# Performance work log

Measured on AMD Instinct MI355X. Metric: run time of the kernel, lower is better.

The kernel has to match this reference:

```python
import jax, jax.numpy as jnp
import numpy as np

N_NODES = 50000
N_EDGES = 1600000
D_IN = 128
D_HID = 128
D_OUT = 128


def setup_inputs() -> dict:
    key = jax.random.key(0)
    ks = jax.random.split(key, 12)
    s = 0.05
    return {
        "x": jax.random.normal(ks[0], (N_NODES, D_IN), jnp.float32),
        "src": jax.random.randint(ks[1], (N_EDGES,), 0, N_NODES),
        "dst": jax.random.randint(ks[2], (N_EDGES,), 0, N_NODES),
        "W_neigh1": jax.random.normal(ks[3], (D_HID, D_IN), jnp.float32) * s,
        "W_self1": jax.random.normal(ks[4], (D_HID, D_IN), jnp.float32) * s,
        "b_self1": jnp.zeros((D_HID,), jnp.float32),
        "W_neigh2": jax.random.normal(ks[5], (D_HID, D_HID), jnp.float32) * s,
        "W_self2": jax.random.normal(ks[6], (D_HID, D_HID), jnp.float32) * s,
        "b_self2": jnp.zeros((D_HID,), jnp.float32),
        "W_neigh3": jax.random.normal(ks[7], (D_OUT, D_HID), jnp.float32) * s,
        "W_self3": jax.random.normal(ks[8], (D_OUT, D_HID), jnp.float32) * s,
        "b_self3": jnp.zeros((D_OUT,), jnp.float32),
    }


def _sage_mean(h, src, dst, inv_deg, W_neigh, W_self, b_self):
    # DGL SAGEConv 'mean': fc_self(h) + fc_neigh(mean of in-neighbor feats)
    # zero in-degree nodes get zero neighbor term (inv_deg = 0 there is avoided
    # by clamping degree to >=1, sum is 0 anyway).
    neigh_sum = jax.ops.segment_sum(h[src], dst, num_segments=h.shape[0])  # [N, d]
    h_neigh = neigh_sum * inv_deg  # [N, d]
    return h @ W_self.T + b_self + h_neigh @ W_neigh.T


def reference(x, src, dst, W_neigh1, W_self1, b_self1, W_neigh2, W_self2, b_self2, W_neigh3, W_self3, b_self3):
    n = x.shape[0]
    deg = jax.ops.segment_sum(jnp.ones((src.shape[0],), x.dtype), dst, num_segments=n)
    inv_deg = (1.0 / jnp.maximum(deg, 1.0))[:, None]  # [N, 1]
    h = jax.nn.relu(_sage_mean(x, src, dst, inv_deg, W_neigh1, W_self1, b_self1))
    h = jax.nn.relu(_sage_mean(h, src, dst, inv_deg, W_neigh2, W_self2, b_self2))
    h = _sage_mean(h, src, dst, inv_deg, W_neigh3, W_self3, b_self3)
    return h
```

## Files before the change

kernel.cpp:

```cpp
#include <hip/hip_runtime.h>


constexpr int N_NODES = 50000;
constexpr int N_EDGES = 1600000;
constexpr int D = 128;

constexpr int NBUCK = 392;
constexpr int BCAP  = 6144;
constexpr int EPB   = 4096;
constexpr int CS_BLOCKS = (N_EDGES + EPB - 1) / EPB;
constexpr int GC_STRIDE = 16;

typedef __bf16 bf16x8 __attribute__((ext_vector_type(8)));
typedef float f32x4 __attribute__((ext_vector_type(4)));
union U8 { bf16x8 v; __bf16 e[8]; };

__global__ void zero1(int* __restrict__ a, int n) {
    int i = blockIdx.x * blockDim.x + threadIdx.x;
    if (i < n) a[i] = 0;
}

__global__ __launch_bounds__(256) void bucket_count_scatter(
        const int* __restrict__ dst, const int* __restrict__ src,
        int* __restrict__ gcursor, int* __restrict__ bucketbuf) {
    __shared__ int hcnt[NBUCK];
    __shared__ int hbase[NBUCK];
    const int tid = threadIdx.x;
    for (int i = tid; i < NBUCK; i += 256) hcnt[i] = 0;
    __syncthreads();

    const int e0 = blockIdx.x * EPB;
    int d[16], lp[16];
    #pragma unroll
    for (int t = 0; t < 16; ++t) {
        const int e = e0 + t * 256 + tid;
        if (e < N_EDGES) {
            d[t] = dst[e];
            lp[t] = atomicAdd(&hcnt[d[t] >> 7], 1);
        } else {
            d[t] = 0; lp[t] = -1;
        }
    }
    __syncthreads();

    for (int i = tid; i < NBUCK; i += 256) {
        const int c = hcnt[i];
        hbase[i] = c ? atomicAdd(&gcursor[i * GC_STRIDE], c) : 0;
    }
    __syncthreads();

    #pragma unroll
    for (int t = 0; t < 16; ++t) {
        const int e = e0 + t * 256 + tid;
        if (e < N_EDGES) {
            const int s  = src[e];
            const int bk = d[t] >> 7;
            const int p  = hbase[bk] + lp[t];
            if (p < BCAP)
                bucketbuf[bk * BCAP + p] = ((d[t] & 127) << 16) | s;
        }
    }
}

__global__ void bucket_scan(const int* __restrict__ gcursor,
                            int* __restrict__ bucket_base,
                            int* __restrict__ row_ptr) {
    __shared__ int wsum[8], wpre[8];
    const int t = threadIdx.x;
    const int lane = t & 63, w = t >> 6;
    int v = 0;
    if (t < NBUCK) { v = gcursor[t * GC_STRIDE]; if (v > BCAP) v = BCAP; }
    int x = v;
    #pragma unroll
    for (int off = 1; off < 64; off <<= 1) {
        int tt = __shfl_up(x, off, 64);
        if (lane >= off) x += tt;
    }
    if (lane == 63) wsum[w] = x;
    __syncthreads();
    if (t < 8) {
        int s = wsum[t], y = s;
        #pragma unroll
        for (int off = 1; off < 8; off <<= 1) {
            int tt = __shfl_up(y, off, 64);
            if (t >= off) y += tt;
        }
        wpre[t] = y - s;
    }
    __syncthreads();
    if (t < NBUCK) bucket_base[t] = wpre[w] + (x - v);
    if (t == 0) row_ptr[N_NODES] = N_EDGES;
}

__global__ __launch_bounds__(256) void bucket_csr(
        const int* __restrict__ gcursor, const int* __restrict__ bucket_base,
        const int* __restrict__ bucketbuf, int* __restrict__ row_ptr,
        float* __restrict__ inv_deg, int* __restrict__ esrc) {
    __shared__ int h[128];
    __shared__ int cur[128];
    __shared__ int s0tot;
    const int bk = blockIdx.x, tid = threadIdx.x;
    int cnt = gcursor[bk * GC_STRIDE];
    if (cnt > BCAP) cnt = BCAP;
    const int base = bucket_base[bk];
    if (tid < 128) h[tid] = 0;
    __syncthreads();

    const int* bb = bucketbuf + (size_t)bk * BCAP;
    for (int i = tid; i < cnt; i += 256) atomicAdd(&h[bb[i] >> 16], 1);
    __syncthreads();

    const int c = (tid < 128) ? h[tid] : 0;
    int x = c;
    const int lane = tid & 63;
    #pragma unroll
    for (int off = 1; off < 64; off <<= 1) {
        int tt = __shfl_up(x, off, 64);
        if (lane >= off) x += tt;
    }
    if (tid == 63) s0tot = x;
    __syncthreads();
    const int excl = x - c + ((tid >= 64 && tid < 128) ? s0tot : 0);
    if (tid < 128) {
        cur[tid] = excl;
        const int node = (bk << 7) + tid;
        if (node < N_NODES) {
            row_ptr[node] = base + excl;
            inv_deg[node] = 1.0f / fmaxf((float)c, 1.0f);
        }
    }
    __syncthreads();

    for (int i = tid; i < cnt; i += 256) {
        const int p = bb[i];
        esrc[base + atomicAdd(&cur[p >> 16], 1)] = p & 0xFFFF;
    }
}

__global__ void pack_w(const float* __restrict__ w0, const float* __restrict__ w1,
                       const float* __restrict__ w2, const float* __restrict__ w3,
                       const float* __restrict__ w4, const float* __restrict__ w5,
                       __bf16* __restrict__ outbase) {
    const float* ws[6] = {w0, w1, w2, w3, w4, w5};
    const float* W = ws[blockIdx.y];
    __bf16* o = outbase + (size_t)blockIdx.y * 32768;
    int idx = blockIdx.x * 256 + threadIdx.x;
    int t = idx & 7;
    int lane = (idx >> 3) & 63;
    int ks = (idx >> 9) & 3;
    int jt = idx >> 11;
    int j = jt * 16 + (lane & 15);
    int k = ks * 32 + (lane >> 4) * 8 + t;
    float w = W[j * D + k];
    __bf16 hi = (__bf16)w;
    o[idx] = hi;
    o[16384 + idx] = (__bf16)(w - (float)hi);
}

__global__ __launch_bounds__(256) void dual_gemm(
        const float* __restrict__ h, const __bf16* __restrict__ Bs,
        const __bf16* __restrict__ Bn, const float* __restrict__ bias,
        float* __restrict__ y_self, __bf16* __restrict__ z) {
    const int wave = threadIdx.x >> 6;
    const int lane = threadIdx.x & 63;
    const int tile = blockIdx.x * 4 + wave;
    if (tile >= N_NODES / 16) return;
    const int n0 = tile * 16;
    const int row = n0 + (lane & 15);
    const int koff = (lane >> 4) * 8;

    U8 ahi[4], alo[4];
    #pragma unroll
    for (int ks = 0; ks < 4; ++ks) {
        const float* p = h + (size_t)row * D + ks * 32 + koff;
        float f[8];
        *(f32x4*)&f[0] = *(const f32x4*)p;
        *(f32x4*)&f[4] = *(const f32x4*)(p + 4);
        #pragma unroll
        for (int t = 0; t < 8; ++t) {
            __bf16 hi = (__bf16)f[t];
            ahi[ks].e[t] = hi;
            alo[ks].e[t] = (__bf16)(f[t] - (float)hi);
        }
    }

    const int jcol = lane & 15;
    const int r0 = (lane >> 4) * 4;

    #pragma unroll 2
    for (int jt = 0; jt < 8; ++jt) {
        f32x4 accS = {0.f, 0.f, 0.f, 0.f};
        f32x4 accN = {0.f, 0.f, 0.f, 0.f};
        #pragma unroll
        for (int ks = 0; ks < 4; ++ks) {
            const size_t off = (((size_t)jt * 4 + ks) * 64 + lane) * 8;
            bf16x8 wsh = *(const bf16x8*)(Bs + off);
            bf16x8 wsl = *(const bf16x8*)(Bs + 16384 + off);
            bf16x8 wnh = *(const bf16x8*)(Bn + off);
            bf16x8 wnl = *(const bf16x8*)(Bn + 16384 + off);
            accS = __builtin_amdgcn_mfma_f32_16x16x32_bf16(ahi[ks].v, wsh, accS, 0, 0, 0);
            accS = __builtin_amdgcn_mfma_f32_16x16x32_bf16(alo[ks].v, wsh, accS, 0, 0, 0);
            accS = __builtin_amdgcn_mfma_f32_16x16x32_bf16(ahi[ks].v, wsl, accS, 0, 0, 0);
            accN = __builtin_amdgcn_mfma_f32_16x16x32_bf16(ahi[ks].v, wnh, accN, 0, 0, 0);
            accN = __builtin_amdgcn_mfma_f32_16x16x32_bf16(alo[ks].v, wnh, accN, 0, 0, 0);
            accN = __builtin_amdgcn_mfma_f32_16x16x32_bf16(ahi[ks].v, wnl, accN, 0, 0, 0);
        }
        const int j = jt * 16 + jcol;
        const float bj = bias[j];
        #pragma unroll
        for (int r = 0; r < 4; ++r) {
            const size_t n = n0 + r0 + r;
            y_self[n * D + j] = accS[r] + bj;
            z[n * D + j] = (__bf16)accN[r];
        }
    }
}

__global__ __launch_bounds__(256) void agg_add(
        const __bf16* __restrict__ z, const int* __restrict__ esrc,
        const int* __restrict__ row_ptr, const float* __restrict__ inv_deg,
        const float* __restrict__ y_self, float* __restrict__ out, int do_relu) {
    const int n = blockIdx.x * 4 + (threadIdx.x >> 6);
    const int lane = threadIdx.x & 63;
    const int s = lane >> 4;
    const int c = lane & 15;
    const int r0 = row_ptr[n], r1 = row_ptr[n + 1];

    float acc[8] = {0.f, 0.f, 0.f, 0.f, 0.f, 0.f, 0.f, 0.f};
    int e = r0 + s;
    for (; e + 12 < r1; e += 16) {
        int i0 = esrc[e], i1 = esrc[e + 4], i2 = esrc[e + 8], i3 = esrc[e + 12];
        U8 v0, v1, v2, v3;
        v0.v = *(const bf16x8*)(z + (size_t)i0 * D + c * 8);
        v1.v = *(const bf16x8*)(z + (size_t)i1 * D + c * 8);
        v2.v = *(const bf16x8*)(z + (size_t)i2 * D + c * 8);
        v3.v = *(const bf16x8*)(z + (size_t)i3 * D + c * 8);
        #pragma unroll
        for (int t = 0; t < 8; ++t)
            acc[t] += ((float)v0.e[t] + (float)v1.e[t]) + ((float)v2.e[t] + (float)v3.e[t]);
    }
    for (; e < r1; e += 4) {
        U8 v0;
        v0.v = *(const bf16x8*)(z + (size_t)esrc[e] * D + c * 8);
        #pragma unroll
        for (int t = 0; t < 8; ++t) acc[t] += (float)v0.e[t];
    }
    #pragma unroll
    for (int t = 0; t < 8; ++t) acc[t] += __shfl_down(acc[t], 32, 64);
    #pragma unroll
    for (int t = 0; t < 8; ++t) acc[t] += __shfl_down(acc[t], 16, 64);

    if (lane < 16) {
        const float idg = inv_deg[n];
        const float* yp = y_self + (size_t)n * D + c * 8;
        f32x4 y0 = *(const f32x4*)yp;
        f32x4 y1 = *(const f32x4*)(yp + 4);
        float o[8];
        #pragma unroll
        for (int t = 0; t < 4; ++t) o[t] = y0[t] + acc[t] * idg;
        #pragma unroll
        for (int t = 0; t < 4; ++t) o[4 + t] = y1[t] + acc[4 + t] * idg;
        if (do_relu) {
            #pragma unroll
            for (int t = 0; t < 8; ++t) o[t] = fmaxf(o[t], 0.f);
        }
        float* op = out + (size_t)n * D + c * 8;
        *(f32x4*)op = *(f32x4*)&o[0];
        *(f32x4*)(op + 4) = *(f32x4*)&o[4];
    }
}

extern "C" void kernel_launch(void* const* d_in, const int* in_sizes, int n_in,
                              void* d_out, int out_size, void* d_ws, size_t ws_size,
                              hipStream_t stream) {
    const float* x   = (const float*)d_in[0];
    const int* src   = (const int*)d_in[1];
    const int* dst   = (const int*)d_in[2];
    const float* Wn1 = (const float*)d_in[3];
    const float* Ws1 = (const float*)d_in[4];
    const float* b1  = (const float*)d_in[5];
    const float* Wn2 = (const float*)d_in[6];
    const float* Ws2 = (const float*)d_in[7];
    const float* b2  = (const float*)d_in[8];
    const float* Wn3 = (const float*)d_in[9];
    const float* Ws3 = (const float*)d_in[10];
    const float* b3  = (const float*)d_in[11];
    float* out = (float*)d_out;

    char* w = (char*)d_ws;
    float* inv_deg     = (float*)w;             w += 50176 * 4;
    int* row_ptr       = (int*)w;               w += 50432 * 4;
    int* gcursor       = (int*)w;               w += NBUCK * GC_STRIDE * 4;
    int* bucket_base   = (int*)w;               w += 512 * 4;
    int* esrc          = (int*)w;               w += (size_t)N_EDGES * 4;
    __bf16* Bpk        = (__bf16*)w;            w += 6 * 32768 * 2;
    __bf16* zbuf       = (__bf16*)w;            w += (size_t)50176 * D * 2;
    float* bufA        = (float*)w;

    int* bucketbuf = (int*)zbuf;

    const __bf16* PWs1 = Bpk + 0 * 32768, *PWn1 = Bpk + 1 * 32768;
    const __bf16* PWs2 = Bpk + 2 * 32768, *PWn2 = Bpk + 3 * 32768;
    const __bf16* PWs3 = Bpk + 4 * 32768, *PWn3 = Bpk + 5 * 32768;

    zero1<<<(NBUCK * GC_STRIDE + 255) / 256, 256, 0, stream>>>(gcursor, NBUCK * GC_STRIDE);
    bucket_count_scatter<<<CS_BLOCKS, 256, 0, stream>>>(dst, src, gcursor, bucketbuf);
    bucket_scan<<<1, 512, 0, stream>>>(gcursor, bucket_base, row_ptr);
    bucket_csr<<<NBUCK, 256, 0, stream>>>(gcursor, bucket_base, bucketbuf,
                                          row_ptr, inv_deg, esrc);

    pack_w<<<dim3(64, 6), 256, 0, stream>>>(Ws1, Wn1, Ws2, Wn2, Ws3, Wn3, Bpk);

    const int ggrid = (N_NODES / 16 + 3) / 4;
    const int agrid = N_NODES / 4;

    dual_gemm<<<ggrid, 256, 0, stream>>>(x, PWs1, PWn1, b1, bufA, zbuf);
    agg_add<<<agrid, 256, 0, stream>>>(zbuf, esrc, row_ptr, inv_deg, bufA, bufA, 1);

    dual_gemm<<<ggrid, 256, 0, stream>>>(bufA, PWs2, PWn2, b2, out, zbuf);
    agg_add<<<agrid, 256, 0, stream>>>(zbuf, esrc, row_ptr, inv_deg, out, out, 1);

    dual_gemm<<<ggrid, 256, 0, stream>>>(out, PWs3, PWn3, b3, bufA, zbuf);
    agg_add<<<agrid, 256, 0, stream>>>(zbuf, esrc, row_ptr, inv_deg, bufA, out, 0);
}
```

Before: 378.9 us.

## Tile neighbor aggregation by source-node range for cache locality

The CSR build now sorts each destination's edges into 8 source-range tiles of 8192 nodes and stores per-(node, tile) offsets instead of a plain row_ptr. The new aggregation kernel loops over the tiles in its outer loop, so all waves gather from the same slice of z at roughly the same time. The aim is for that slice to stay cache-resident and cut random HBM traffic. Each wave now handles 14 nodes with half-waves and a fixed grid of 1024 blocks. In exchange there are many short divergent per-tile loops and fewer waves in flight.

```diff
diff --git a/kernel.cpp b/kernel.cpp
--- a/kernel.cpp
+++ b/kernel.cpp
@@ -10,6 +10,11 @@
 constexpr int EPB   = 4096;
 constexpr int CS_BLOCKS = (N_EDGES + EPB - 1) / EPB;
 constexpr int GC_STRIDE = 16;
+
+constexpr int NT  = 8;
+constexpr int TSH = 13;
+constexpr int AGG_BLOCKS = 1024;
+constexpr int PW = 14;
 
 typedef __bf16 bf16x8 __attribute__((ext_vector_type(8)));
 typedef float f32x4 __attribute__((ext_vector_type(4)));
@@ -63,8 +68,7 @@
 }
 
 __global__ void bucket_scan(const int* __restrict__ gcursor,
-                            int* __restrict__ bucket_base,
-                            int* __restrict__ row_ptr) {
+                            int* __restrict__ bucket_base) {
     __shared__ int wsum[8], wpre[8];
     const int t = threadIdx.x;
     const int lane = t & 63, w = t >> 6;
@@ -89,51 +93,66 @@
     }
     __syncthreads();
     if (t < NBUCK) bucket_base[t] = wpre[w] + (x - v);
-    if (t == 0) row_ptr[N_NODES] = N_EDGES;
 }
 
 __global__ __launch_bounds__(256) void bucket_csr(
         const int* __restrict__ gcursor, const int* __restrict__ bucket_base,
-        const int* __restrict__ bucketbuf, int* __restrict__ row_ptr,
+        const int* __restrict__ bucketbuf, int* __restrict__ tp,
         float* __restrict__ inv_deg, int* __restrict__ esrc) {
-    __shared__ int h[128];
-    __shared__ int cur[128];
-    __shared__ int s0tot;
+    __shared__ int h[1024];
+    __shared__ int cur[1024];
+    __shared__ int wsum[4], wpre[4];
     const int bk = blockIdx.x, tid = threadIdx.x;
     int cnt = gcursor[bk * GC_STRIDE];
     if (cnt > BCAP) cnt = BCAP;
     const int base = bucket_base[bk];
-    if (tid < 128) h[tid] = 0;
+    #pragma unroll
+    for (int k = 0; k < 4; ++k) h[tid * 4 + k] = 0;
     __syncthreads();
 
     const int* bb = bucketbuf + (size_t)bk * BCAP;
-    for (int i = tid; i < cnt; i += 256) atomicAdd(&h[bb[i] >> 16], 1);
-    __syncthreads();
-
-    const int c = (tid < 128) ? h[tid] : 0;
-    int x = c;
-    const int lane = tid & 63;
+    for (int i = tid; i < cnt; i += 256) {
+        const int p = bb[i];
+        atomicAdd(&h[((p >> 16) << 3) | ((p & 0xFFFF) >> TSH)], 1);
+    }
+    __syncthreads();
+
+    if (tid < 128) {
+        int dg = 0;
+        #pragma unroll
+        for (int k = 0; k < 8; ++k) dg += h[tid * 8 + k];
+        inv_deg[bk * 128 + tid] = 1.0f / fmaxf((float)dg, 1.0f);
+    }
+
+    int v0 = h[tid * 4], v1 = h[tid * 4 + 1], v2 = h[tid * 4 + 2], v3 = h[tid * 4 + 3];
+    const int s = v0 + v1 + v2 + v3;
+    int x = s;
+    const int lane = tid & 63, w = tid >> 6;
     #pragma unroll
     for (int off = 1; off < 64; off <<= 1) {
         int tt = __shfl_up(x, off, 64);
         if (lane >= off) x += tt;
     }
-    if (tid == 63) s0tot = x;
-    __syncthreads();
-    const int excl = x - c + ((tid >= 64 && tid < 128) ? s0tot : 0);
-    if (tid < 128) {
-        cur[tid] = excl;
-        const int node = (bk << 7) + tid;
-        if (node < N_NODES) {
-            row_ptr[node] = base + excl;
-            inv_deg[node] = 1.0f / fmaxf((float)c, 1.0f);
-        }
-    }
+    if (lane == 63) wsum[w] = x;
+    __syncthreads();
+    if (tid == 0) {
+        int a = 0;
+        #pragma unroll
+        for (int k = 0; k < 4; ++k) { wpre[k] = a; a += wsum[k]; }
+    }
+    __syncthreads();
+    const int e0 = wpre[w] + (x - s);
+    const int e1 = e0 + v0, e2 = e1 + v1, e3 = e2 + v2;
+    cur[tid * 4] = e0; cur[tid * 4 + 1] = e1;
+    cur[tid * 4 + 2] = e2; cur[tid * 4 + 3] = e3;
+    int* tpo = tp + (size_t)bk * 1024 + tid * 4;
+    tpo[0] = base + e0; tpo[1] = base + e1; tpo[2] = base + e2; tpo[3] = base + e3;
     __syncthreads();
 
     for (int i = tid; i < cnt; i += 256) {
         const int p = bb[i];
-        esrc[base + atomicAdd(&cur[p >> 16], 1)] = p & 0xFFFF;
+        const int f = ((p >> 16) << 3) | ((p & 0xFFFF) >> TSH);
+        esrc[base + atomicAdd(&cur[f], 1)] = p & 0xFFFF;
     }
 }
 
@@ -216,57 +235,70 @@
     }
 }
 
-__global__ __launch_bounds__(256) void agg_add(
+__global__ __launch_bounds__(256, 4) void agg_tiled(
         const __bf16* __restrict__ z, const int* __restrict__ esrc,
-        const int* __restrict__ row_ptr, const float* __restrict__ inv_deg,
+        const int* __restrict__ tp, const float* __restrict__ inv_deg,
         const float* __restrict__ y_self, float* __restrict__ out, int do_relu) {
-    const int n = blockIdx.x * 4 + (threadIdx.x >> 6);
+    const int wid = (blockIdx.x * 256 + threadIdx.x) >> 6;
     const int lane = threadIdx.x & 63;
-    const int s = lane >> 4;
-    const int c = lane & 15;
-    const int r0 = row_ptr[n], r1 = row_ptr[n + 1];
-
-    float acc[8] = {0.f, 0.f, 0.f, 0.f, 0.f, 0.f, 0.f, 0.f};
-    int e = r0 + s;
-    for (; e + 12 < r1; e += 16) {
-        int i0 = esrc[e], i1 = esrc[e + 4], i2 = esrc[e + 8], i3 = esrc[e + 12];
-        U8 v0, v1, v2, v3;
-        v0.v = *(const bf16x8*)(z + (size_t)i0 * D + c * 8);
-        v1.v = *(const bf16x8*)(z + (size_t)i1 * D + c * 8);
-        v2.v = *(const bf16x8*)(z + (size_t)i2 * D + c * 8);
-        v3.v = *(const bf16x8*)(z + (size_t)i3 * D + c * 8);
-        #pragma unroll
-        for (int t = 0; t < 8; ++t)
-            acc[t] += ((float)v0.e[t] + (float)v1.e[t]) + ((float)v2.e[t] + (float)v3.e[t]);
-    }
-    for (; e < r1; e += 4) {
-        U8 v0;
-        v0.v = *(const bf16x8*)(z + (size_t)esrc[e] * D + c * 8);
-        #pragma unroll
-        for (int t = 0; t < 8; ++t) acc[t] += (float)v0.e[t];
-    }
-    #pragma unroll
-    for (int t = 0; t < 8; ++t) acc[t] += __shfl_down(acc[t], 32, 64);
-    #pragma unroll
-    for (int t = 0; t < 8; ++t) acc[t] += __shfl_down(acc[t], 16, 64);
-
-    if (lane < 16) {
-        const float idg = inv_deg[n];
-        const float* yp = y_self + (size_t)n * D + c * 8;
-        f32x4 y0 = *(const f32x4*)yp;
-        f32x4 y1 = *(const f32x4*)(yp + 4);
-        float o[8];
-        #pragma unroll
-        for (int t = 0; t < 4; ++t) o[t] = y0[t] + acc[t] * idg;
-        #pragma unroll
-        for (int t = 0; t < 4; ++t) o[4 + t] = y1[t] + acc[4 + t] * idg;
-        if (do_relu) {
+    const int half = lane >> 5;
+    const int hl = lane & 31;
+
+    f32x4 acc[7];
+    #pragma unroll
+    for (int i = 0; i < 7; ++i) acc[i] = (f32x4){0.f, 0.f, 0.f, 0.f};
+
+    const char* zc = (const char*)z;
+    const unsigned coff = (unsigned)hl * 8u;
+
+    for (int t = 0; t < NT; ++t) {
+        #pragma unroll
+        for (int pi = 0; pi < 7; ++pi) {
+            const int n = (pi * 2 + half) * 4096 + wid;
+            int r0 = 0, r1 = 0;
+            if (n < N_NODES) {
+                r0 = tp[n * NT + t];
+                r1 = tp[n * NT + t + 1];
+            }
+            int e = r0;
+            while (__any(e < r1)) {
+                if (e < r1) {
+                    const unsigned s = (unsigned)esrc[e];
+                    const uint2 v = *(const uint2*)(zc + (size_t)s * 256u + coff);
+                    acc[pi][0] += __uint_as_float(v.x << 16);
+                    acc[pi][1] += __uint_as_float(v.x & 0xffff0000u);
+                    acc[pi][2] += __uint_as_float(v.y << 16);
+                    acc[pi][3] += __uint_as_float(v.y & 0xffff0000u);
+                }
+                if (e + 1 < r1) {
+                    const unsigned s = (unsigned)esrc[e + 1];
+                    const uint2 v = *(const uint2*)(zc + (size_t)s * 256u + coff);
+                    acc[pi][0] += __uint_as_float(v.x << 16);
+                    acc[pi][1] += __uint_as_float(v.x & 0xffff0000u);
+                    acc[pi][2] += __uint_as_float(v.y << 16);
+                    acc[pi][3] += __uint_as_float(v.y & 0xffff0000u);
+                }
+                e += 2;
+            }
+        }
+    }
+
+    #pragma unroll
+    for (int pi = 0; pi < 7; ++pi) {
+        const int n = (pi * 2 + half) * 4096 + wid;
+        if (n < N_NODES) {
+            const float idg = inv_deg[n];
+            const float* yp = y_self + (size_t)n * D + hl * 4;
+            const f32x4 y = *(const f32x4*)yp;
+            f32x4 o;
             #pragma unroll
-            for (int t = 0; t < 8; ++t) o[t] = fmaxf(o[t], 0.f);
-        }
-        float* op = out + (size_t)n * D + c * 8;
-        *(f32x4*)op = *(f32x4*)&o[0];
-        *(f32x4*)(op + 4) = *(f32x4*)&o[4];
+            for (int k = 0; k < 4; ++k) o[k] = y[k] + acc[pi][k] * idg;
+            if (do_relu) {
+                #pragma unroll
+                for (int k = 0; k < 4; ++k) o[k] = fmaxf(o[k], 0.f);
+            }
+            *(f32x4*)(out + (size_t)n * D + hl * 4) = o;
+        }
     }
 }
 
@@ -289,7 +321,7 @@
 
     char* w = (char*)d_ws;
     float* inv_deg     = (float*)w;             w += 50176 * 4;
-    int* row_ptr       = (int*)w;               w += 50432 * 4;
+    int* tp            = (int*)w;               w += (size_t)NBUCK * 1024 * 4;
     int* gcursor       = (int*)w;               w += NBUCK * GC_STRIDE * 4;
     int* bucket_base   = (int*)w;               w += 512 * 4;
     int* esrc          = (int*)w;               w += (size_t)N_EDGES * 4;
@@ -305,21 +337,20 @@
 
     zero1<<<(NBUCK * GC_STRIDE + 255) / 256, 256, 0, stream>>>(gcursor, NBUCK * GC_STRIDE);
     bucket_count_scatter<<<CS_BLOCKS, 256, 0, stream>>>(dst, src, gcursor, bucketbuf);
-    bucket_scan<<<1, 512, 0, stream>>>(gcursor, bucket_base, row_ptr);
+    bucket_scan<<<1, 512, 0, stream>>>(gcursor, bucket_base);
     bucket_csr<<<NBUCK, 256, 0, stream>>>(gcursor, bucket_base, bucketbuf,
-                                          row_ptr, inv_deg, esrc);
+                                          tp, inv_deg, esrc);
 
     pack_w<<<dim3(64, 6), 256, 0, stream>>>(Ws1, Wn1, Ws2, Wn2, Ws3, Wn3, Bpk);
 
     const int ggrid = (N_NODES / 16 + 3) / 4;
-    const int agrid = N_NODES / 4;
 
     dual_gemm<<<ggrid, 256, 0, stream>>>(x, PWs1, PWn1, b1, bufA, zbuf);
-    agg_add<<<agrid, 256, 0, stream>>>(zbuf, esrc, row_ptr, inv_deg, bufA, bufA, 1);
+    agg_tiled<<<AGG_BLOCKS, 256, 0, stream>>>(zbuf, esrc, tp, inv_deg, bufA, bufA, 1);
 
     dual_gemm<<<ggrid, 256, 0, stream>>>(bufA, PWs2, PWn2, b2, out, zbuf);
-    agg_add<<<agrid, 256, 0, stream>>>(zbuf, esrc, row_ptr, inv_deg, out, out, 1);
+    agg_tiled<<<AGG_BLOCKS, 256, 0, stream>>>(zbuf, esrc, tp, inv_deg, out, out, 1);
 
     dual_gemm<<<ggrid, 256, 0, stream>>>(out, PWs3, PWn3, b3, bufA, zbuf);
-    agg_add<<<agrid, 256, 0, stream>>>(zbuf, esrc, row_ptr, inv_deg, bufA, out, 0);
-}
+    agg_tiled<<<AGG_BLOCKS, 256, 0, stream>>>(zbuf, esrc, tp, inv_deg, bufA, out, 0);
+}
```

After: 744.6 us. 96.5% more time.

## Sort each node's edges by source-range tile for gather locality

Applied to the files above, without the earlier changes.

The CSR build now bins each destination's edges into 8 sub-buckets keyed by source index high bits, giving a per-node order sorted by source tile. A 1024-entry per-bucket tile-pointer array replaces row_ptr, and aggregation reads row bounds from it with stride NT. The aim is better L2 locality for the bf16 feature gathers, since concurrently running nodes hit similar source ranges. The cost is larger shared histograms and scan work in bucket_csr, plus the tp[(n+1)*NT] read at the last node relying on the padded bucket layout.

```diff
diff --git a/kernel.cpp b/kernel.cpp
--- a/kernel.cpp
+++ b/kernel.cpp
@@ -10,6 +10,9 @@
 constexpr int EPB   = 4096;
 constexpr int CS_BLOCKS = (N_EDGES + EPB - 1) / EPB;
 constexpr int GC_STRIDE = 16;
+
+constexpr int NT  = 8;
+constexpr int TSH = 13;
 
 typedef __bf16 bf16x8 __attribute__((ext_vector_type(8)));
 typedef float f32x4 __attribute__((ext_vector_type(4)));
@@ -63,8 +66,7 @@
 }
 
 __global__ void bucket_scan(const int* __restrict__ gcursor,
-                            int* __restrict__ bucket_base,
-                            int* __restrict__ row_ptr) {
+                            int* __restrict__ bucket_base) {
     __shared__ int wsum[8], wpre[8];
     const int t = threadIdx.x;
     const int lane = t & 63, w = t >> 6;
@@ -89,51 +91,67 @@
     }
     __syncthreads();
     if (t < NBUCK) bucket_base[t] = wpre[w] + (x - v);
-    if (t == 0) row_ptr[N_NODES] = N_EDGES;
 }
 
 __global__ __launch_bounds__(256) void bucket_csr(
         const int* __restrict__ gcursor, const int* __restrict__ bucket_base,
-        const int* __restrict__ bucketbuf, int* __restrict__ row_ptr,
+        const int* __restrict__ bucketbuf, int* __restrict__ tp,
         float* __restrict__ inv_deg, int* __restrict__ esrc) {
-    __shared__ int h[128];
-    __shared__ int cur[128];
-    __shared__ int s0tot;
+    __shared__ int h[1024];
+    __shared__ int cur[1024];
+    __shared__ int wsum[4], wpre[4];
     const int bk = blockIdx.x, tid = threadIdx.x;
     int cnt = gcursor[bk * GC_STRIDE];
     if (cnt > BCAP) cnt = BCAP;
     const int base = bucket_base[bk];
-    if (tid < 128) h[tid] = 0;
+    #pragma unroll
+    for (int k = 0; k < 4; ++k) h[tid * 4 + k] = 0;
     __syncthreads();
 
     const int* bb = bucketbuf + (size_t)bk * BCAP;
-    for (int i = tid; i < cnt; i += 256) atomicAdd(&h[bb[i] >> 16], 1);
-    __syncthreads();
-
-    const int c = (tid < 128) ? h[tid] : 0;
-    int x = c;
-    const int lane = tid & 63;
+    for (int i = tid; i < cnt; i += 256) {
+        const int p = bb[i];
+        atomicAdd(&h[((p >> 16) << 3) | ((p & 0xFFFF) >> TSH)], 1);
+    }
+    __syncthreads();
+
+    if (tid < 128) {
+        int dg = 0;
+        #pragma unroll
+        for (int k = 0; k < 8; ++k) dg += h[tid * 8 + k];
+        inv_deg[bk * 128 + tid] = 1.0f / fmaxf((float)dg, 1.0f);
+    }
+
+    const int v0 = h[tid * 4], v1 = h[tid * 4 + 1];
+    const int v2 = h[tid * 4 + 2], v3 = h[tid * 4 + 3];
+    const int s = v0 + v1 + v2 + v3;
+    int x = s;
+    const int lane = tid & 63, w = tid >> 6;
     #pragma unroll
     for (int off = 1; off < 64; off <<= 1) {
         int tt = __shfl_up(x, off, 64);
         if (lane >= off) x += tt;
     }
-    if (tid == 63) s0tot = x;
-    __syncthreads();
-    const int excl = x - c + ((tid >= 64 && tid < 128) ? s0tot : 0);
-    if (tid < 128) {
-        cur[tid] = excl;
-        const int node = (bk << 7) + tid;
-        if (node < N_NODES) {
-            row_ptr[node] = base + excl;
-            inv_deg[node] = 1.0f / fmaxf((float)c, 1.0f);
-        }
-    }
+    if (lane == 63) wsum[w] = x;
+    __syncthreads();
+    if (tid == 0) {
+        int a = 0;
+        #pragma unroll
+        for (int k = 0; k < 4; ++k) { wpre[k] = a; a += wsum[k]; }
+    }
+    __syncthreads();
+    const int e0 = wpre[w] + (x - s);
+    const int e1 = e0 + v0, e2 = e1 + v1, e3 = e2 + v2;
+    cur[tid * 4] = e0; cur[tid * 4 + 1] = e1;
+    cur[tid * 4 + 2] = e2; cur[tid * 4 + 3] = e3;
+    int* tpo = tp + (size_t)bk * 1024 + tid * 4;
+    tpo[0] = base + e0; tpo[1] = base + e1; tpo[2] = base + e2; tpo[3] = base + e3;
     __syncthreads();
 
     for (int i = tid; i < cnt; i += 256) {
         const int p = bb[i];
-        esrc[base + atomicAdd(&cur[p >> 16], 1)] = p & 0xFFFF;
+        const int f = ((p >> 16) << 3) | ((p & 0xFFFF) >> TSH);
+        esrc[base + atomicAdd(&cur[f], 1)] = p & 0xFFFF;
     }
 }
 
@@ -218,13 +236,13 @@
 
 __global__ __launch_bounds__(256) void agg_add(
         const __bf16* __restrict__ z, const int* __restrict__ esrc,
-        const int* __restrict__ row_ptr, const float* __restrict__ inv_deg,
+        const int* __restrict__ tp, const float* __restrict__ inv_deg,
         const float* __restrict__ y_self, float* __restrict__ out, int do_relu) {
     const int n = blockIdx.x * 4 + (threadIdx.x >> 6);
     const int lane = threadIdx.x & 63;
     const int s = lane >> 4;
     const int c = lane & 15;
-    const int r0 = row_ptr[n], r1 = row_ptr[n + 1];
+    const int r0 = tp[n * NT], r1 = tp[(n + 1) * NT];
 
     float acc[8] = {0.f, 0.f, 0.f, 0.f, 0.f, 0.f, 0.f, 0.f};
     int e = r0 + s;
@@ -289,7 +307,7 @@
 
     char* w = (char*)d_ws;
     float* inv_deg     = (float*)w;             w += 50176 * 4;
-    int* row_ptr       = (int*)w;               w += 50432 * 4;
+    int* tp            = (int*)w;               w += (size_t)NBUCK * 1024 * 4;
     int* gcursor       = (int*)w;               w += NBUCK * GC_STRIDE * 4;
     int* bucket_base   = (int*)w;               w += 512 * 4;
     int* esrc          = (int*)w;               w += (size_t)N_EDGES * 4;
@@ -305,9 +323,9 @@
 
     zero1<<<(NBUCK * GC_STRIDE + 255) / 256, 256, 0, stream>>>(gcursor, NBUCK * GC_STRIDE);
     bucket_count_scatter<<<CS_BLOCKS, 256, 0, stream>>>(dst, src, gcursor, bucketbuf);
-    bucket_scan<<<1, 512, 0, stream>>>(gcursor, bucket_base, row_ptr);
+    bucket_scan<<<1, 512, 0, stream>>>(gcursor, bucket_base);
     bucket_csr<<<NBUCK, 256, 0, stream>>>(gcursor, bucket_base, bucketbuf,
-                                          row_ptr, inv_deg, esrc);
+                                          tp, inv_deg, esrc);
 
     pack_w<<<dim3(64, 6), 256, 0, stream>>>(Ws1, Wn1, Ws2, Wn2, Ws3, Wn3, Bpk);
 
@@ -315,11 +333,11 @@
     const int agrid = N_NODES / 4;
 
     dual_gemm<<<ggrid, 256, 0, stream>>>(x, PWs1, PWn1, b1, bufA, zbuf);
-    agg_add<<<agrid, 256, 0, stream>>>(zbuf, esrc, row_ptr, inv_deg, bufA, bufA, 1);
+    agg_add<<<agrid, 256, 0, stream>>>(zbuf, esrc, tp, inv_deg, bufA, bufA, 1);
 
     dual_gemm<<<ggrid, 256, 0, stream>>>(bufA, PWs2, PWn2, b2, out, zbuf);
-    agg_add<<<agrid, 256, 0, stream>>>(zbuf, esrc, row_ptr, inv_deg, out, out, 1);
+    agg_add<<<agrid, 256, 0, stream>>>(zbuf, esrc, tp, inv_deg, out, out, 1);
 
     dual_gemm<<<ggrid, 256, 0, stream>>>(out, PWs3, PWn3, b3, bufA, zbuf);
-    agg_add<<<agrid, 256, 0, stream>>>(zbuf, esrc, row_ptr, inv_deg, bufA, out, 0);
-}
+    agg_add<<<agrid, 256, 0, stream>>>(zbuf, esrc, tp, inv_deg, bufA, out, 0);
+}
```

New measurement: 380.7 us (median of 2 runs). No clear change (+0.5%).
